# Kernel optimization log

Measured on AMD Instinct MI355X. Metric: run time of the kernel, lower is better.

## Reference

```python
import jax, jax.numpy as jnp
import numpy as np
from math import sqrt

B, S, D_MODEL, H, DK, DV = 16, 512, 256, 8, 32, 32
EPS = 1e-5


def layer_norm(x, g, b):
    m = jnp.mean(x, axis=-1, keepdims=True)
    v = jnp.mean((x - m) ** 2, axis=-1, keepdims=True)
    return g * (x - m) / jnp.sqrt(v + EPS) + b


def setup_inputs() -> dict:
    key = jax.random.key(0)
    ks = jax.random.split(key, 16)
    inp = {
        "input_Q": jax.random.normal(ks[0], (B, S, D_MODEL), jnp.float32),
        "input_K": jax.random.normal(ks[1], (B, S, D_MODEL), jnp.float32),
        "input_V": jax.random.normal(ks[2], (B, S, D_MODEL), jnp.float32),
        "attn_mask": jax.random.bernoulli(ks[3], 0.1, (B, H, S, S)),
        "matrix": jax.random.uniform(ks[4], (B, S, S), jnp.float32),
        # learned params (stored [in, out], i.e. transpose of torch Linear weight)
        "W_Q": jax.random.normal(ks[5], (D_MODEL, H * DK), jnp.float32) * 0.02,
        "W_K": jax.random.normal(ks[6], (D_MODEL, H * DK), jnp.float32) * 0.02,
        "W_V": jax.random.normal(ks[7], (D_MODEL, H * DV), jnp.float32) * 0.02,
        "W_V2": jax.random.normal(ks[8], (D_MODEL, DV), jnp.float32) * 0.02,
        "W_fc": jax.random.normal(ks[9], (DV * (H + 1), D_MODEL), jnp.float32) * 0.02,
        "ln_g": jnp.ones((D_MODEL,), jnp.float32),
        "ln_b": jnp.zeros((D_MODEL,), jnp.float32),
        "fu_ln_g": jnp.ones((H + 1,), jnp.float32),
        "fu_ln_b": jnp.zeros((H + 1,), jnp.float32),
        "fu_w1": jax.random.normal(ks[10], (H + 1, 6), jnp.float32) * 0.3,
        "fu_b1": jnp.zeros((6,), jnp.float32),
        "fu_w2": jax.random.normal(ks[11], (6, 1), jnp.float32) * 0.3,
        "fu_b2": jnp.zeros((1,), jnp.float32),
    }
    return inp


def reference(input_Q, input_K, input_V, attn_mask, matrix,
              W_Q, W_K, W_V, W_V2, W_fc, ln_g, ln_b,
              fu_ln_g, fu_ln_b, fu_w1, fu_b1, fu_w2, fu_b2):
    b = input_Q.shape[0]
    # project and split heads: [B, H, S, d]
    Q = (input_Q @ W_Q).reshape(b, -1, H, DK).transpose(0, 2, 1, 3)
    K = (input_K @ W_K).reshape(b, -1, H, DK).transpose(0, 2, 1, 3)
    V = (input_V @ W_V).reshape(b, -1, H, DV).transpose(0, 2, 1, 3)
    scores = jnp.einsum('bhqd,bhkd->bhqk', Q, K) / sqrt(DK)
    scores = jnp.where(attn_mask, -1e9, scores)
    attn = jax.nn.softmax(scores, axis=-1)            # [B, H, S, S]
    context = jnp.einsum('bhqk,bhkd->bhqd', attn, V)  # [B, H, S, DV]
    # second context from pairwise matrix
    context2 = matrix @ (input_V @ W_V2)              # [B, S, DV]
    # gated matrix update: concat matrix with attn maps along head axis
    gate_in = jnp.concatenate([matrix[:, None], attn], axis=1)  # [B, H+1, S, S]
    gate_in = gate_in.transpose(0, 3, 2, 1)                     # [B, S, S, H+1]
    g = layer_norm(gate_in, fu_ln_g, fu_ln_b)
    g = jax.nn.relu(g @ fu_w1 + fu_b1)
    g = jax.nn.sigmoid(g @ fu_w2 + fu_b2)[..., 0]               # [B, S, S]
    matrix_out = matrix * g
    # merge heads, concat, project, layernorm
    context = context.transpose(0, 2, 1, 3).reshape(b, -1, H * DV)
    context = jnp.concatenate([context, context2], axis=-1)     # [B, S, DV*(H+1)]
    output = layer_norm(context @ W_fc, ln_g, ln_b)
    return (output, matrix_out)
```

## Files before the change

kernel.cpp:

```cpp
#include <hip/hip_runtime.h>
#include <hip/hip_bf16.h>

#define BB 16
#define SS 512
#define DM 256
#define NH 8

#define OFF_QB    0
#define OFF_KB    1048576
#define OFF_VT    2097152
#define OFF_VP2   3145728
#define OFF_CTXB  3407872
#define OFF_CTX2B 4456448
#define OFF_G     4587520
#define OFF_FLAG  6684672
#define OFF_PM    6684674

#define SCALE 0.17677669529663687f

typedef __attribute__((ext_vector_type(8))) short bfrag8;
typedef __attribute__((ext_vector_type(4))) float facc4;

__global__ void mask_or_kernel(const unsigned int* __restrict__ w,
                               unsigned int* __restrict__ acc) {
  __shared__ unsigned int sh[256];
  unsigned int a = 0;
  int base = blockIdx.x * 1024;
  for (int i = threadIdx.x; i < 1024; i += 256) a |= w[base + i];
  sh[threadIdx.x] = a;
  __syncthreads();
  for (int s = 128; s > 0; s >>= 1) {
    if (threadIdx.x < s) sh[threadIdx.x] |= sh[threadIdx.x + s];
    __syncthreads();
  }
  if (threadIdx.x == 0) atomicOr(acc, sh[0]);
}

__global__ __launch_bounds__(256) void mask_pack_kernel(
    const void* __restrict__ mask, unsigned long long* __restrict__ pm,
    const unsigned int* __restrict__ orv) {
  const unsigned int rawor = *orv;
  const int flagv = (rawor <= 1u) ? 0 : ((rawor == 0x3F800000u) ? 2 : 1);
  const int lane = threadIdx.x & 63;
  const int wv = threadIdx.x >> 6;
  const int w0 = (blockIdx.x * 4 + wv) * 32;
  const unsigned char* mb = (const unsigned char*)mask;
  const int* mi = (const int*)mask;
  const float* mf = (const float*)mask;
  unsigned long long myw = 0;
#pragma unroll 4
  for (int i = 0; i < 32; i++) {
    long long idx = (long long)(w0 + i) * 64 + lane;
    bool m;
    if (flagv == 1) m = (mb[idx] != 0);
    else if (flagv == 0) m = (mi[idx] != 0);
    else m = (mf[idx] != 0.f);
    unsigned long long bits = __ballot(m);
    if (lane == i) myw = bits;
  }
  if (lane < 32) pm[w0 + lane] = myw;
}

__global__ __launch_bounds__(256) void gemm_qkv_kernel(
    const float* __restrict__ inQ, const float* __restrict__ inK,
    const float* __restrict__ inV,
    const float* __restrict__ Wq, const float* __restrict__ Wk,
    const float* __restrict__ Wv,
    __hip_bfloat16* __restrict__ Qb, __hip_bfloat16* __restrict__ Kb,
    __hip_bfloat16* __restrict__ Vt) {
  __shared__ __align__(16) __hip_bfloat16 As[64][40];
  __shared__ __align__(16) __hip_bfloat16 Bs[64][40];
  const int tid = threadIdx.x;
  const int bid = blockIdx.x;
  const int matid = bid >> 9;
  const int mblk = (bid & 511) >> 2;
  const int nblk = bid & 3;
  const int m0 = mblk * 64;
  const int n0 = nblk * 64;
  const float* X = (matid == 0) ? inQ : (matid == 1) ? inK : inV;
  const float* W = (matid == 0) ? Wq : (matid == 1) ? Wk : Wv;

  const int lane = tid & 63;
  const int w = tid >> 6;
  const int wm = w & 1, wn = w >> 1;
  const int cl = lane & 15, quad = lane >> 4;
  const int arow = tid >> 2, ak8 = (tid & 3) * 8;
  const int bn = tid & 63, bk8 = (tid >> 6) * 8;

  facc4 acc[2][2];
#pragma unroll
  for (int t = 0; t < 2; t++)
#pragma unroll
    for (int u = 0; u < 2; u++) acc[t][u] = (facc4){0.f, 0.f, 0.f, 0.f};

#pragma unroll 1
  for (int kc = 0; kc < 8; kc++) {
    float4 x0 = *(const float4*)&X[(m0 + arow) * 256 + kc * 32 + ak8];
    float4 x1 = *(const float4*)&X[(m0 + arow) * 256 + kc * 32 + ak8 + 4];
    float wv[8];
#pragma unroll
    for (int j = 0; j < 8; j++) wv[j] = W[(kc * 32 + bk8 + j) * 256 + n0 + bn];
    __syncthreads();
    {
      __hip_bfloat16 ta[8];
      ta[0] = __float2bfloat16(x0.x); ta[1] = __float2bfloat16(x0.y);
      ta[2] = __float2bfloat16(x0.z); ta[3] = __float2bfloat16(x0.w);
      ta[4] = __float2bfloat16(x1.x); ta[5] = __float2bfloat16(x1.y);
      ta[6] = __float2bfloat16(x1.z); ta[7] = __float2bfloat16(x1.w);
      *(uint4*)&As[arow][ak8] = *(uint4*)ta;
      __hip_bfloat16 tb[8];
#pragma unroll
      for (int j = 0; j < 8; j++) tb[j] = __float2bfloat16(wv[j]);
      *(uint4*)&Bs[bn][bk8] = *(uint4*)tb;
    }
    __syncthreads();
    bfrag8 aA[2], bB[2];
#pragma unroll
    for (int t = 0; t < 2; t++)
      aA[t] = *(const bfrag8*)&As[wm * 32 + t * 16 + cl][quad * 8];
#pragma unroll
    for (int u = 0; u < 2; u++)
      bB[u] = *(const bfrag8*)&Bs[wn * 32 + u * 16 + cl][quad * 8];
#pragma unroll
    for (int t = 0; t < 2; t++)
#pragma unroll
      for (int u = 0; u < 2; u++)
        acc[t][u] =
            __builtin_amdgcn_mfma_f32_16x16x32_bf16(aA[t], bB[u], acc[t][u], 0, 0, 0);
  }

  if (matid < 2) {
    __hip_bfloat16* Y = (matid == 0) ? Qb : Kb;
#pragma unroll
    for (int t = 0; t < 2; t++)
#pragma unroll
      for (int u = 0; u < 2; u++)
#pragma unroll
        for (int reg = 0; reg < 4; reg++)
          Y[(m0 + wm * 32 + t * 16 + quad * 4 + reg) * 256 + n0 + wn * 32 +
            u * 16 + cl] = __float2bfloat16(acc[t][u][reg]);
  } else {
#pragma unroll
    for (int t = 0; t < 2; t++)
#pragma unroll
      for (int u = 0; u < 2; u++) {
        int c = n0 + wn * 32 + u * 16 + cl;
        int mg = m0 + wm * 32 + t * 16 + quad * 4;
        int b = mg >> 9, s = mg & 511;
        __hip_bfloat16 pk[4];
#pragma unroll
        for (int reg = 0; reg < 4; reg++)
          pk[reg] = __float2bfloat16(acc[t][u][reg]);
        *(ushort4*)&Vt[(((b << 8) + c) << 9) + s] = *(ushort4*)pk;
      }
  }
}

__global__ __launch_bounds__(256) void vp2_kernel(
    const float* __restrict__ inV, const float* __restrict__ Wv2,
    float* __restrict__ Vp2) {
  __shared__ __align__(16) float xs[16][260];
  const int t = threadIdx.x;
  const int r0 = blockIdx.x * 16;
  for (int e = t; e < 16 * 256; e += 256) {
    int r = e >> 8, i = e & 255;
    xs[r][i] = inV[(r0 + r) * 256 + i];
  }
  __syncthreads();
  const int c2 = t & 31, rr = t >> 5;
  float a0 = 0.f, a1 = 0.f;
  for (int i = 0; i < 256; i += 4) {
    float w0 = Wv2[i * 32 + c2], w1 = Wv2[(i + 1) * 32 + c2];
    float w2 = Wv2[(i + 2) * 32 + c2], w3 = Wv2[(i + 3) * 32 + c2];
    float4 xa = *(const float4*)&xs[rr][i];
    float4 xb = *(const float4*)&xs[rr + 8][i];
    a0 += xa.x * w0 + xa.y * w1 + xa.z * w2 + xa.w * w3;
    a1 += xb.x * w0 + xb.y * w1 + xb.z * w2 + xb.w * w3;
  }
  Vp2[(r0 + rr) * 32 + c2] = a0;
  Vp2[(r0 + rr + 8) * 32 + c2] = a1;
}

__global__ __launch_bounds__(512) void attn_kernel(
    const __hip_bfloat16* __restrict__ Qb, const __hip_bfloat16* __restrict__ Kb,
    const __hip_bfloat16* __restrict__ Vt,
    const unsigned long long* __restrict__ pm,
    const float* __restrict__ matrix,
    const float* __restrict__ fulng, const float* __restrict__ fulnb,
    const float* __restrict__ fuw1, const float* __restrict__ fub1,
    const float* __restrict__ fuw2, const float* __restrict__ fub2,
    __hip_bfloat16* __restrict__ ctxb, __hip_bfloat16* __restrict__ gws) {
  __shared__ __align__(16) __hip_bfloat16 Sb[NH][16][136];
  __shared__ float fup[85];

  const int tid = threadIdx.x;
  const int lane = tid & 63;
  const int h = tid >> 6;
  const int cl = lane & 15, quad = lane >> 4;
  const int b = ((blockIdx.x & 7) << 1) | (blockIdx.x >> 8);
  const int q0 = ((blockIdx.x >> 3) & 31) * 16;

  if (tid < 9) fup[tid] = fulng[tid];
  else if (tid < 18) fup[tid] = fulnb[tid - 9];
  else if (tid < 72) fup[tid] = fuw1[tid - 18];
  else if (tid < 78) fup[tid] = fub1[tid - 72];
  else if (tid < 84) fup[tid] = fuw2[tid - 78];
  else if (tid == 84) fup[tid] = fub2[0];

  const unsigned long long* pmb = pm + (((b * NH + h) << 9) + q0) * 8;

  const bfrag8 aQ =
      *(const bfrag8*)&Qb[(((b << 9) + q0 + cl) << 8) + h * 32 + quad * 8];
  const __hip_bfloat16* KbB = &Kb[((b << 9) << 8) + h * 32 + quad * 8];
  const __hip_bfloat16* VtB = &Vt[(((b << 8) + h * 32) << 9)];

  float mx[4] = {-3e38f, -3e38f, -3e38f, -3e38f};
#pragma unroll 4
  for (int nt = 0; nt < 32; nt++) {
    bfrag8 bK = *(const bfrag8*)&KbB[(nt * 16 + cl) << 8];
    facc4 cc = {0.f, 0.f, 0.f, 0.f};
    cc = __builtin_amdgcn_mfma_f32_16x16x32_bf16(aQ, bK, cc, 0, 0, 0);
#pragma unroll
    for (int r = 0; r < 4; r++) mx[r] = fmaxf(mx[r], cc[r]);
  }
#pragma unroll
  for (int r = 0; r < 4; r++)
#pragma unroll
    for (int off = 1; off <= 8; off <<= 1)
      mx[r] = fmaxf(mx[r], __shfl_xor(mx[r], off));

  float l[4] = {0.f, 0.f, 0.f, 0.f};
#pragma unroll 2
  for (int w8 = 0; w8 < 8; w8++) {
    unsigned long long mw[4];
#pragma unroll
    for (int r = 0; r < 4; r++)
      mw[r] = pmb[(quad * 4 + r) * 8 + w8] >> cl;
#pragma unroll
    for (int n4 = 0; n4 < 4; n4++) {
      const int nt = w8 * 4 + n4;
      bfrag8 bK = *(const bfrag8*)&KbB[(nt * 16 + cl) << 8];
      facc4 cc = {0.f, 0.f, 0.f, 0.f};
      cc = __builtin_amdgcn_mfma_f32_16x16x32_bf16(aQ, bK, cc, 0, 0, 0);
#pragma unroll
      for (int r = 0; r < 4; r++) {
        float e = ((mw[r] >> (n4 * 16)) & 1ULL)
                      ? 0.f
                      : __expf(SCALE * (cc[r] - mx[r]));
        l[r] += e;
      }
    }
  }
#pragma unroll
  for (int r = 0; r < 4; r++)
#pragma unroll
    for (int off = 1; off <= 8; off <<= 1) l[r] += __shfl_xor(l[r], off);
  float invl[4];
#pragma unroll
  for (int r = 0; r < 4; r++) invl[r] = 1.f / l[r];

  facc4 a0 = {0.f, 0.f, 0.f, 0.f}, a1 = {0.f, 0.f, 0.f, 0.f};
#pragma unroll 1
  for (int c = 0; c < 4; c++) {
    if (c) __syncthreads();
#pragma unroll
    for (int w8 = c * 2; w8 < c * 2 + 2; w8++) {
      unsigned long long mw[4];
#pragma unroll
      for (int r = 0; r < 4; r++)
        mw[r] = pmb[(quad * 4 + r) * 8 + w8] >> cl;
#pragma unroll
      for (int n4 = 0; n4 < 4; n4++) {
        const int nt = w8 * 4 + n4;
        bfrag8 bK = *(const bfrag8*)&KbB[(nt * 16 + cl) << 8];
        facc4 cc = {0.f, 0.f, 0.f, 0.f};
        cc = __builtin_amdgcn_mfma_f32_16x16x32_bf16(aQ, bK, cc, 0, 0, 0);
#pragma unroll
        for (int r = 0; r < 4; r++) {
          float e = ((mw[r] >> (n4 * 16)) & 1ULL)
                        ? 0.f
                        : __expf(SCALE * (cc[r] - mx[r]));
          Sb[h][quad * 4 + r][nt * 16 + cl - c * 128] =
              __float2bfloat16(e * invl[r]);
        }
      }
    }
    __syncthreads();

    {
      const int gq = tid >> 5;
      const int k4 = (tid & 31) * 4;
      float4 mrow =
          *(const float4*)&matrix[((b << 9) + q0 + gq) * 512 + c * 128 + k4];
      float p[NH][4];
#pragma unroll
      for (int hh = 0; hh < NH; hh++) {
        ushort4 sv = *(const ushort4*)&Sb[hh][gq][k4];
        p[hh][0] = __bfloat162float(*(__hip_bfloat16*)&sv.x);
        p[hh][1] = __bfloat162float(*(__hip_bfloat16*)&sv.y);
        p[hh][2] = __bfloat162float(*(__hip_bfloat16*)&sv.z);
        p[hh][3] = __bfloat162float(*(__hip_bfloat16*)&sv.w);
      }
      const float mcomp[4] = {mrow.x, mrow.y, mrow.z, mrow.w};
      __hip_bfloat16 gout[4];
#pragma unroll
      for (int i = 0; i < 4; i++) {
        float v[9];
        v[0] = mcomp[i];
#pragma unroll
        for (int t = 0; t < NH; t++) v[1 + t] = p[t][i];
        float mu = 0.f;
#pragma unroll
        for (int t = 0; t < 9; t++) mu += v[t];
        mu *= (1.f / 9.f);
        float var = 0.f;
#pragma unroll
        for (int t = 0; t < 9; t++) {
          float d = v[t] - mu;
          var += d * d;
        }
        var *= (1.f / 9.f);
        float inv = rsqrtf(var + 1e-5f);
        float y[9];
#pragma unroll
        for (int t = 0; t < 9; t++)
          y[t] = fup[t] * (v[t] - mu) * inv + fup[9 + t];
        float o = fup[84];
#pragma unroll
        for (int j = 0; j < 6; j++) {
          float z = fup[72 + j];
#pragma unroll
          for (int t = 0; t < 9; t++) z += y[t] * fup[18 + t * 6 + j];
          z = fmaxf(z, 0.f);
          o += z * fup[78 + j];
        }
        gout[i] = __float2bfloat16(1.f / (1.f + __expf(-o)));
      }
      *(ushort4*)&gws[((b << 9) + q0 + gq) * 512 + c * 128 + k4] =
          *(ushort4*)gout;
    }

#pragma unroll
    for (int ks = 0; ks < 4; ks++) {
      bfrag8 aP = *(const bfrag8*)&Sb[h][cl][ks * 32 + quad * 8];
      bfrag8 b0 =
          *(const bfrag8*)&VtB[(cl << 9) + c * 128 + ks * 32 + quad * 8];
      bfrag8 b1 =
          *(const bfrag8*)&VtB[((16 + cl) << 9) + c * 128 + ks * 32 + quad * 8];
      a0 = __builtin_amdgcn_mfma_f32_16x16x32_bf16(aP, b0, a0, 0, 0, 0);
      a1 = __builtin_amdgcn_mfma_f32_16x16x32_bf16(aP, b1, a1, 0, 0, 0);
    }
  }

#pragma unroll
  for (int r = 0; r < 4; r++) {
    int row = quad * 4 + r;
    ctxb[((b << 9) + q0 + row) * 256 + h * 32 + cl] = __float2bfloat16(a0[r]);
    ctxb[((b << 9) + q0 + row) * 256 + h * 32 + 16 + cl] =
        __float2bfloat16(a1[r]);
  }
}

__global__ __launch_bounds__(256) void mout_kernel(
    const float* __restrict__ matrix, const __hip_bfloat16* __restrict__ g,
    float* __restrict__ mout) {
  __shared__ float Gs[64][65];
  const int tid = threadIdx.x;
  const int b = blockIdx.x >> 6;
  const int j0 = ((blockIdx.x >> 3) & 7) * 64;
  const int i0 = (blockIdx.x & 7) * 64;

  {
    int r = tid >> 2, c0 = (tid & 3) * 16;
    const __hip_bfloat16* gp = g + (((b << 9) + i0 + r) << 9) + j0 + c0;
    ushort us[16];
    *(uint4*)(us) = *(const uint4*)(gp);
    *(uint4*)(us + 8) = *(const uint4*)(gp + 8);
#pragma unroll
    for (int k = 0; k < 16; k++) {
      __hip_bfloat16 hv = *(__hip_bfloat16*)&us[k];
      Gs[r][c0 + k] = __bfloat162float(hv);
    }
  }
  __syncthreads();

  {
    int jj = tid >> 2, ic = (tid & 3) * 16;
    const float* mp = matrix + (((b << 9) + j0 + jj) << 9) + i0 + ic;
    float* op = mout + (((b << 9) + j0 + jj) << 9) + i0 + ic;
#pragma unroll
    for (int v4 = 0; v4 < 4; v4++) {
      float4 m = *(const float4*)(mp + v4 * 4);
      float4 o;
      o.x = m.x * Gs[ic + v4 * 4 + 0][jj];
      o.y = m.y * Gs[ic + v4 * 4 + 1][jj];
      o.z = m.z * Gs[ic + v4 * 4 + 2][jj];
      o.w = m.w * Gs[ic + v4 * 4 + 3][jj];
      *(float4*)(op + v4 * 4) = o;
    }
  }
}

__global__ __launch_bounds__(256) void ctx2_kernel(
    const float* __restrict__ matrix, const float* __restrict__ Vp2,
    __hip_bfloat16* __restrict__ ctx2b) {
  __shared__ __align__(16) float Ms[16][128];
  __shared__ __align__(16) float Vs2t[32][132];
  const int t = threadIdx.x;
  const int b = blockIdx.x >> 5;
  const int s0 = (blockIdx.x & 31) * 16;
  const int dv = t & 31, rg = t >> 5;
  float acc0 = 0.f, acc1 = 0.f;
  for (int kc = 0; kc < 4; kc++) {
    __syncthreads();
#pragma unroll
    for (int it = 0; it < 8; it++) {
      int idx = t + it * 256;
      int r = idx >> 7, cc = idx & 127;
      Ms[r][cc] = matrix[((b << 9) + s0 + r) * 512 + kc * 128 + cc];
    }
#pragma unroll
    for (int it = 0; it < 16; it++) {
      int e = t + it * 256;
      int k = e >> 5, dv2 = e & 31;
      Vs2t[dv2][k] = Vp2[((b << 9) + kc * 128 + k) * 32 + dv2];
    }
    __syncthreads();
    for (int k = 0; k < 128; k += 4) {
      float4 vv = *(const float4*)&Vs2t[dv][k];
      float4 m0 = *(const float4*)&Ms[rg][k];
      float4 m1 = *(const float4*)&Ms[rg + 8][k];
      acc0 += m0.x * vv.x + m0.y * vv.y + m0.z * vv.z + m0.w * vv.w;
      acc1 += m1.x * vv.x + m1.y * vv.y + m1.z * vv.z + m1.w * vv.w;
    }
  }
  ctx2b[((b << 9) + s0 + rg) * 32 + dv] = __float2bfloat16(acc0);
  ctx2b[((b << 9) + s0 + rg + 8) * 32 + dv] = __float2bfloat16(acc1);
}

__global__ __launch_bounds__(256) void final_kernel(
    const __hip_bfloat16* __restrict__ ctxb,
    const __hip_bfloat16* __restrict__ ctx2b, const float* __restrict__ Wfc,
    const float* __restrict__ lng, const float* __restrict__ lnb,
    float* __restrict__ out) {
  __shared__ __align__(16) __hip_bfloat16 As[32][40];
  __shared__ __align__(16) __hip_bfloat16 Bs[256][40];
  __shared__ __align__(16) float xs[32][260];
  __shared__ float red2[32][8][2];
  __shared__ float musig[32][2];
  const int tid = threadIdx.x;
  const int m0 = blockIdx.x * 32;
  const int lane = tid & 63, w = tid >> 6;
  const int cl = lane & 15, quad = lane >> 4;
  const int arow = tid >> 3, ak4 = (tid & 7) * 4;

  facc4 acc[2][4];
#pragma unroll
  for (int t = 0; t < 2; t++)
#pragma unroll
    for (int u = 0; u < 4; u++) acc[t][u] = (facc4){0.f, 0.f, 0.f, 0.f};

#pragma unroll 1
  for (int kc = 0; kc < 9; kc++) {
    ushort4 av;
    if (kc < 8)
      av = *(const ushort4*)&ctxb[(m0 + arow) * 256 + kc * 32 + ak4];
    else
      av = *(const ushort4*)&ctx2b[(m0 + arow) * 32 + ak4];
    float wv[32];
#pragma unroll
    for (int j = 0; j < 32; j++) wv[j] = Wfc[(kc * 32 + j) * 256 + tid];
    __syncthreads();
    *(ushort4*)&As[arow][ak4] = av;
    {
      __hip_bfloat16 tw[32];
#pragma unroll
      for (int j = 0; j < 32; j++) tw[j] = __float2bfloat16(wv[j]);
#pragma unroll
      for (int g = 0; g < 4; g++) *(uint4*)&Bs[tid][g * 8] = *(uint4*)&tw[g * 8];
    }
    __syncthreads();
    bfrag8 aA[2], bB[4];
#pragma unroll
    for (int t = 0; t < 2; t++)
      aA[t] = *(const bfrag8*)&As[t * 16 + cl][quad * 8];
#pragma unroll
    for (int u = 0; u < 4; u++)
      bB[u] = *(const bfrag8*)&Bs[w * 64 + u * 16 + cl][quad * 8];
#pragma unroll
    for (int t = 0; t < 2; t++)
#pragma unroll
      for (int u = 0; u < 4; u++)
        acc[t][u] =
            __builtin_amdgcn_mfma_f32_16x16x32_bf16(aA[t], bB[u], acc[t][u], 0, 0, 0);
  }

#pragma unroll
  for (int t = 0; t < 2; t++)
#pragma unroll
    for (int u = 0; u < 4; u++)
#pragma unroll
      for (int reg = 0; reg < 4; reg++)
        xs[t * 16 + quad * 4 + reg][w * 64 + u * 16 + cl] = acc[t][u][reg];
  __syncthreads();

  {
    int r = tid >> 3, c0 = (tid & 7) * 32;
    float s1 = 0.f, s2 = 0.f;
    for (int j = 0; j < 32; j += 4) {
      float4 v = *(const float4*)&xs[r][c0 + j];
      s1 += v.x + v.y + v.z + v.w;
      s2 += v.x * v.x + v.y * v.y + v.z * v.z + v.w * v.w;
    }
    red2[r][tid & 7][0] = s1;
    red2[r][tid & 7][1] = s2;
  }
  __syncthreads();
  if (tid < 32) {
    float s1 = 0.f, s2 = 0.f;
#pragma unroll
    for (int j = 0; j < 8; j++) {
      s1 += red2[tid][j][0];
      s2 += red2[tid][j][1];
    }
    float mu = s1 * (1.f / 256.f);
    float var = s2 * (1.f / 256.f) - mu * mu;
    musig[tid][0] = mu;
    musig[tid][1] = rsqrtf(var + 1e-5f);
  }
  __syncthreads();
  {
    float gt = lng[tid], bt = lnb[tid];
#pragma unroll 4
    for (int r = 0; r < 32; r++)
      out[(m0 + r) * 256 + tid] =
          gt * (xs[r][tid] - musig[r][0]) * musig[r][1] + bt;
  }
}

extern "C" void kernel_launch(void* const* d_in, const int* in_sizes, int n_in,
                              void* d_out, int out_size, void* d_ws,
                              size_t ws_size, hipStream_t stream) {
  const float* inQ = (const float*)d_in[0];
  const float* inK = (const float*)d_in[1];
  const float* inV = (const float*)d_in[2];
  const void* mask = d_in[3];
  const float* matrix = (const float*)d_in[4];
  const float* Wq = (const float*)d_in[5];
  const float* Wk = (const float*)d_in[6];
  const float* Wv = (const float*)d_in[7];
  const float* Wv2 = (const float*)d_in[8];
  const float* Wfc = (const float*)d_in[9];
  const float* lng = (const float*)d_in[10];
  const float* lnb = (const float*)d_in[11];
  const float* fulng = (const float*)d_in[12];
  const float* fulnb = (const float*)d_in[13];
  const float* fuw1 = (const float*)d_in[14];
  const float* fub1 = (const float*)d_in[15];
  const float* fuw2 = (const float*)d_in[16];
  const float* fub2 = (const float*)d_in[17];

  float* ws = (float*)d_ws;
  __hip_bfloat16* Qb = (__hip_bfloat16*)(ws + OFF_QB);
  __hip_bfloat16* Kb = (__hip_bfloat16*)(ws + OFF_KB);
  __hip_bfloat16* Vt = (__hip_bfloat16*)(ws + OFF_VT);
  float* Vp2 = ws + OFF_VP2;
  __hip_bfloat16* ctxb = (__hip_bfloat16*)(ws + OFF_CTXB);
  __hip_bfloat16* ctx2b = (__hip_bfloat16*)(ws + OFF_CTX2B);
  __hip_bfloat16* gws = (__hip_bfloat16*)(ws + OFF_G);
  unsigned int* flag = (unsigned int*)(ws + OFF_FLAG);
  unsigned long long* pmask = (unsigned long long*)(ws + OFF_PM);

  float* out = (float*)d_out;
  float* mout = out + BB * SS * DM;

  hipMemsetAsync(flag, 0, 4, stream);
  mask_or_kernel<<<64, 256, 0, stream>>>((const unsigned int*)mask, flag);
  mask_pack_kernel<<<4096, 256, 0, stream>>>(mask, pmask, flag);
  gemm_qkv_kernel<<<1536, 256, 0, stream>>>(inQ, inK, inV, Wq, Wk, Wv, Qb, Kb,
                                            Vt);
  vp2_kernel<<<512, 256, 0, stream>>>(inV, Wv2, Vp2);
  attn_kernel<<<512, 512, 0, stream>>>(Qb, Kb, Vt, pmask, matrix, fulng, fulnb,
                                       fuw1, fub1, fuw2, fub2, ctxb, gws);
  mout_kernel<<<BB * 64, 256, 0, stream>>>(matrix, gws, mout);
  ctx2_kernel<<<512, 256, 0, stream>>>(matrix, Vp2, ctx2b);
  final_kernel<<<256, 256, 0, stream>>>(ctxb, ctx2b, Wfc, lng, lnb, out);
}
```

Baseline: 410.9 us.

## Drop max pass, single-pass QK with deferred normalization and folded gate MLP

Removes the separate row-max pass by computing exp2 of prescaled scores directly, computes QK once while storing unnormalised probabilities for the full row in shared memory, then does PV in one loop and applies 1/l at the output. Gate LayerNorm is rewritten with sum/sum-of-squares and its affine params folded into the first MLP layer. Shared memory grows a lot, lowering occupancy, and skipping max subtraction risks overflow for large scores.

Result: faster. 386.6 us (-5.9%).

```diff
diff --git a/kernel.cpp b/kernel.cpp
--- a/kernel.cpp
+++ b/kernel.cpp
@@ -17,6 +17,7 @@
 #define OFF_PM    6684674
 
 #define SCALE 0.17677669529663687f
+#define KE2 0.2550348623f
 
 typedef __attribute__((ext_vector_type(8))) short bfrag8;
 typedef __attribute__((ext_vector_type(4))) float facc4;
@@ -181,7 +182,7 @@
   Vp2[(r0 + rr + 8) * 32 + c2] = a1;
 }
 
-__global__ __launch_bounds__(512) void attn_kernel(
+__global__ __launch_bounds__(512, 2) void attn_kernel(
     const __hip_bfloat16* __restrict__ Qb, const __hip_bfloat16* __restrict__ Kb,
     const __hip_bfloat16* __restrict__ Vt,
     const unsigned long long* __restrict__ pm,
@@ -190,8 +191,9 @@
     const float* __restrict__ fuw1, const float* __restrict__ fub1,
     const float* __restrict__ fuw2, const float* __restrict__ fub2,
     __hip_bfloat16* __restrict__ ctxb, __hip_bfloat16* __restrict__ gws) {
-  __shared__ __align__(16) __hip_bfloat16 Sb[NH][16][136];
-  __shared__ float fup[85];
+  __shared__ __align__(16) __hip_bfloat16 Sb[NH][16][520];
+  __shared__ float inv_s[NH][16];
+  __shared__ float gp[80];
 
   const int tid = threadIdx.x;
   const int lane = tid & 63;
@@ -200,12 +202,22 @@
   const int b = ((blockIdx.x & 7) << 1) | (blockIdx.x >> 8);
   const int q0 = ((blockIdx.x >> 3) & 31) * 16;
 
-  if (tid < 9) fup[tid] = fulng[tid];
-  else if (tid < 18) fup[tid] = fulnb[tid - 9];
-  else if (tid < 72) fup[tid] = fuw1[tid - 18];
-  else if (tid < 78) fup[tid] = fub1[tid - 72];
-  else if (tid < 84) fup[tid] = fuw2[tid - 78];
-  else if (tid == 84) fup[tid] = fub2[0];
+  if (tid < 6) {
+    const int j = tid;
+    float s1 = 0.f, c1 = fub1[j];
+#pragma unroll
+    for (int t = 0; t < 9; t++) {
+      float w = fuw1[t * 6 + j];
+      float gw = fulng[t] * w;
+      gp[t * 6 + j] = gw;
+      s1 += gw;
+      c1 += fulnb[t] * w;
+    }
+    gp[54 + j] = s1;
+    gp[60 + j] = c1;
+    gp[66 + j] = fuw2[j];
+    if (j == 0) gp[72] = fub2[0];
+  }
 
   const unsigned long long* pmb = pm + (((b * NH + h) << 9) + q0) * 8;
 
@@ -213,21 +225,6 @@
       *(const bfrag8*)&Qb[(((b << 9) + q0 + cl) << 8) + h * 32 + quad * 8];
   const __hip_bfloat16* KbB = &Kb[((b << 9) << 8) + h * 32 + quad * 8];
   const __hip_bfloat16* VtB = &Vt[(((b << 8) + h * 32) << 9)];
-
-  float mx[4] = {-3e38f, -3e38f, -3e38f, -3e38f};
-#pragma unroll 4
-  for (int nt = 0; nt < 32; nt++) {
-    bfrag8 bK = *(const bfrag8*)&KbB[(nt * 16 + cl) << 8];
-    facc4 cc = {0.f, 0.f, 0.f, 0.f};
-    cc = __builtin_amdgcn_mfma_f32_16x16x32_bf16(aQ, bK, cc, 0, 0, 0);
-#pragma unroll
-    for (int r = 0; r < 4; r++) mx[r] = fmaxf(mx[r], cc[r]);
-  }
-#pragma unroll
-  for (int r = 0; r < 4; r++)
-#pragma unroll
-    for (int off = 1; off <= 8; off <<= 1)
-      mx[r] = fmaxf(mx[r], __shfl_xor(mx[r], off));
 
   float l[4] = {0.f, 0.f, 0.f, 0.f};
 #pragma unroll 2
@@ -244,10 +241,9 @@
       cc = __builtin_amdgcn_mfma_f32_16x16x32_bf16(aQ, bK, cc, 0, 0, 0);
 #pragma unroll
       for (int r = 0; r < 4; r++) {
-        float e = ((mw[r] >> (n4 * 16)) & 1ULL)
-                      ? 0.f
-                      : __expf(SCALE * (cc[r] - mx[r]));
+        float e = ((mw[r] >> (n4 * 16)) & 1ULL) ? 0.f : exp2f(KE2 * cc[r]);
         l[r] += e;
+        Sb[h][quad * 4 + r][nt * 16 + cl] = __float2bfloat16(e);
       }
     }
   }
@@ -258,48 +254,39 @@
   float invl[4];
 #pragma unroll
   for (int r = 0; r < 4; r++) invl[r] = 1.f / l[r];
+  if (cl == 0) {
+#pragma unroll
+    for (int r = 0; r < 4; r++) inv_s[h][quad * 4 + r] = invl[r];
+  }
+  __syncthreads();
 
   facc4 a0 = {0.f, 0.f, 0.f, 0.f}, a1 = {0.f, 0.f, 0.f, 0.f};
+#pragma unroll 4
+  for (int ks = 0; ks < 16; ks++) {
+    bfrag8 aP = *(const bfrag8*)&Sb[h][cl][ks * 32 + quad * 8];
+    bfrag8 b0 = *(const bfrag8*)&VtB[(cl << 9) + ks * 32 + quad * 8];
+    bfrag8 b1 = *(const bfrag8*)&VtB[((16 + cl) << 9) + ks * 32 + quad * 8];
+    a0 = __builtin_amdgcn_mfma_f32_16x16x32_bf16(aP, b0, a0, 0, 0, 0);
+    a1 = __builtin_amdgcn_mfma_f32_16x16x32_bf16(aP, b1, a1, 0, 0, 0);
+  }
+
+  {
+    const int gq = tid >> 5;
+    const int g32 = (tid & 31) * 4;
 #pragma unroll 1
-  for (int c = 0; c < 4; c++) {
-    if (c) __syncthreads();
-#pragma unroll
-    for (int w8 = c * 2; w8 < c * 2 + 2; w8++) {
-      unsigned long long mw[4];
-#pragma unroll
-      for (int r = 0; r < 4; r++)
-        mw[r] = pmb[(quad * 4 + r) * 8 + w8] >> cl;
-#pragma unroll
-      for (int n4 = 0; n4 < 4; n4++) {
-        const int nt = w8 * 4 + n4;
-        bfrag8 bK = *(const bfrag8*)&KbB[(nt * 16 + cl) << 8];
-        facc4 cc = {0.f, 0.f, 0.f, 0.f};
-        cc = __builtin_amdgcn_mfma_f32_16x16x32_bf16(aQ, bK, cc, 0, 0, 0);
-#pragma unroll
-        for (int r = 0; r < 4; r++) {
-          float e = ((mw[r] >> (n4 * 16)) & 1ULL)
-                        ? 0.f
-                        : __expf(SCALE * (cc[r] - mx[r]));
-          Sb[h][quad * 4 + r][nt * 16 + cl - c * 128] =
-              __float2bfloat16(e * invl[r]);
-        }
-      }
-    }
-    __syncthreads();
-
-    {
-      const int gq = tid >> 5;
-      const int k4 = (tid & 31) * 4;
+    for (int s = 0; s < 4; s++) {
+      const int k4 = s * 128 + g32;
       float4 mrow =
-          *(const float4*)&matrix[((b << 9) + q0 + gq) * 512 + c * 128 + k4];
+          *(const float4*)&matrix[((b << 9) + q0 + gq) * 512 + k4];
       float p[NH][4];
 #pragma unroll
       for (int hh = 0; hh < NH; hh++) {
+        const float iv = inv_s[hh][gq];
         ushort4 sv = *(const ushort4*)&Sb[hh][gq][k4];
-        p[hh][0] = __bfloat162float(*(__hip_bfloat16*)&sv.x);
-        p[hh][1] = __bfloat162float(*(__hip_bfloat16*)&sv.y);
-        p[hh][2] = __bfloat162float(*(__hip_bfloat16*)&sv.z);
-        p[hh][3] = __bfloat162float(*(__hip_bfloat16*)&sv.w);
+        p[hh][0] = __bfloat162float(*(__hip_bfloat16*)&sv.x) * iv;
+        p[hh][1] = __bfloat162float(*(__hip_bfloat16*)&sv.y) * iv;
+        p[hh][2] = __bfloat162float(*(__hip_bfloat16*)&sv.z) * iv;
+        p[hh][3] = __bfloat162float(*(__hip_bfloat16*)&sv.w) * iv;
       }
       const float mcomp[4] = {mrow.x, mrow.y, mrow.z, mrow.w};
       __hip_bfloat16 gout[4];
@@ -309,55 +296,38 @@
         v[0] = mcomp[i];
 #pragma unroll
         for (int t = 0; t < NH; t++) v[1 + t] = p[t][i];
-        float mu = 0.f;
-#pragma unroll
-        for (int t = 0; t < 9; t++) mu += v[t];
-        mu *= (1.f / 9.f);
-        float var = 0.f;
+        float s1 = 0.f, s2 = 0.f;
 #pragma unroll
         for (int t = 0; t < 9; t++) {
-          float d = v[t] - mu;
-          var += d * d;
+          s1 += v[t];
+          s2 += v[t] * v[t];
         }
-        var *= (1.f / 9.f);
+        float mu = s1 * (1.f / 9.f);
+        float var = s2 * (1.f / 9.f) - mu * mu;
         float inv = rsqrtf(var + 1e-5f);
-        float y[9];
-#pragma unroll
-        for (int t = 0; t < 9; t++)
-          y[t] = fup[t] * (v[t] - mu) * inv + fup[9 + t];
-        float o = fup[84];
+        float o = gp[72];
 #pragma unroll
         for (int j = 0; j < 6; j++) {
-          float z = fup[72 + j];
-#pragma unroll
-          for (int t = 0; t < 9; t++) z += y[t] * fup[18 + t * 6 + j];
+          float d = 0.f;
+#pragma unroll
+          for (int t = 0; t < 9; t++) d += v[t] * gp[t * 6 + j];
+          float z = inv * (d - mu * gp[54 + j]) + gp[60 + j];
           z = fmaxf(z, 0.f);
-          o += z * fup[78 + j];
+          o += z * gp[66 + j];
         }
         gout[i] = __float2bfloat16(1.f / (1.f + __expf(-o)));
       }
-      *(ushort4*)&gws[((b << 9) + q0 + gq) * 512 + c * 128 + k4] =
-          *(ushort4*)gout;
-    }
-
-#pragma unroll
-    for (int ks = 0; ks < 4; ks++) {
-      bfrag8 aP = *(const bfrag8*)&Sb[h][cl][ks * 32 + quad * 8];
-      bfrag8 b0 =
-          *(const bfrag8*)&VtB[(cl << 9) + c * 128 + ks * 32 + quad * 8];
-      bfrag8 b1 =
-          *(const bfrag8*)&VtB[((16 + cl) << 9) + c * 128 + ks * 32 + quad * 8];
-      a0 = __builtin_amdgcn_mfma_f32_16x16x32_bf16(aP, b0, a0, 0, 0, 0);
-      a1 = __builtin_amdgcn_mfma_f32_16x16x32_bf16(aP, b1, a1, 0, 0, 0);
+      *(ushort4*)&gws[((b << 9) + q0 + gq) * 512 + k4] = *(ushort4*)gout;
     }
   }
 
 #pragma unroll
   for (int r = 0; r < 4; r++) {
     int row = quad * 4 + r;
-    ctxb[((b << 9) + q0 + row) * 256 + h * 32 + cl] = __float2bfloat16(a0[r]);
+    ctxb[((b << 9) + q0 + row) * 256 + h * 32 + cl] =
+        __float2bfloat16(a0[r] * invl[r]);
     ctxb[((b << 9) + q0 + row) * 256 + h * 32 + 16 + cl] =
-        __float2bfloat16(a1[r]);
+        __float2bfloat16(a1[r] * invl[r]);
   }
 }
 
```
